# Kernel optimization log

Measured on AMD Instinct MI355X. Metric: run time of the kernel, lower is better.

## Reference

```python
import jax, jax.numpy as jnp
import numpy as np

N = 500_000   # active voxel sites
C = 128       # inplanes == outplanes
K = 4         # 2x2 submanifold filter offsets
EPS = 1e-4    # SCN BatchNorm default eps


def setup_inputs() -> dict:
    key = jax.random.key(0)
    ks = jax.random.split(key, 10)
    feat = jax.random.normal(ks[0], (N, C), jnp.float32)
    in_idx = jax.random.randint(ks[1], (K, N), 0, N, dtype=jnp.int32)
    out_idx = jax.random.randint(ks[2], (K, N), 0, N, dtype=jnp.int32)
    mask = jax.random.randint(ks[3], (K, N), 0, 2, dtype=jnp.int32)
    scale = 1.0 / np.sqrt(K * C)
    W1 = jax.random.normal(ks[4], (K, C, C), jnp.float32) * scale
    W2 = jax.random.normal(ks[5], (K, C, C), jnp.float32) * scale
    gamma1 = jnp.ones((C,), jnp.float32)
    beta1 = jnp.zeros((C,), jnp.float32)
    mean1 = jax.random.normal(ks[6], (C,), jnp.float32) * 0.1
    var1 = jax.random.uniform(ks[7], (C,), jnp.float32, 0.5, 1.5)
    gamma2 = jnp.ones((C,), jnp.float32)
    beta2 = jnp.zeros((C,), jnp.float32)
    mean2 = jax.random.normal(ks[8], (C,), jnp.float32) * 0.1
    var2 = jax.random.uniform(ks[9], (C,), jnp.float32, 0.5, 1.5)
    return dict(feat=feat, W1=W1, W2=W2, gamma1=gamma1, beta1=beta1,
                mean1=mean1, var1=var1, gamma2=gamma2, beta2=beta2,
                mean2=mean2, var2=var2, in_idx=in_idx, out_idx=out_idx, mask=mask)


def _subm_conv(feat, W, in_idx, out_idx, maskf):
    # rulebook gather -> GEMM -> scatter-add, one pass per kernel offset
    out = jnp.zeros((feat.shape[0], W.shape[-1]), feat.dtype)
    for k in range(W.shape[0]):  # K=4 fixed small offsets
        g = feat[in_idx[k]] * maskf[k][:, None]   # [N, Cin]
        out = out.at[out_idx[k]].add(g @ W[k])    # scatter to active sites
    return out


def _bn(x, gamma, beta, mean, var):
    return (x - mean) * jax.lax.rsqrt(var + EPS) * gamma + beta


def reference(feat, W1, W2, gamma1, beta1, mean1, var1,
              gamma2, beta2, mean2, var2, in_idx, out_idx, mask):
    maskf = mask.astype(feat.dtype)
    residual = feat                              # scn.Identity (stride=1)
    h = _subm_conv(feat, W1, in_idx, out_idx, maskf)
    h = jax.nn.relu(_bn(h, gamma1, beta1, mean1, var1))  # BatchNormReLU
    h = _subm_conv(h, W2, in_idx, out_idx, maskf)
    h = _bn(h, gamma2, beta2, mean2, var2)       # BatchNormalization
    return h + residual                          # AddTable
```

## Files before the change

kernel.cpp:

```cpp
#include <hip/hip_runtime.h>

#define CDIM 128
#define KOFF 4
#define EPS 1e-4f
#define SCAN_CHUNK 2048
#define ROWS 16
#define NBUF 4
#define NBLK 512
#define NTHR 512
#define CAPM (1 << 18)

typedef __attribute__((ext_vector_type(8))) short bf16x8;
typedef __attribute__((ext_vector_type(4))) float f32x4;

__device__ __forceinline__ unsigned short f2bf(float f) {
    unsigned int u = __builtin_bit_cast(unsigned int, f);
    u += 0x7fffu + ((u >> 16) & 1u);
    return (unsigned short)(u >> 16);
}
__device__ __forceinline__ float bf2f(unsigned short h) {
    unsigned int u = ((unsigned int)h) << 16;
    return __builtin_bit_cast(float, u);
}

__device__ __forceinline__ void gload_lds16(const void* g, void* l) {
    __builtin_amdgcn_global_load_lds(
        (const __attribute__((address_space(1))) void*)g,
        (__attribute__((address_space(3))) void*)l, 16, 0, 0);
}

__global__ __launch_bounds__(256) void wconv_kernel(
    const float* __restrict__ W1, const float* __restrict__ W2,
    short* __restrict__ W1t, short* __restrict__ W2t)
{
    int idx = blockIdx.x * 256 + threadIdx.x;
    if (idx >= KOFF * CDIM * CDIM) return;
    int ci = idx & (CDIM - 1);
    int co = (idx >> 7) & (CDIM - 1);
    int k  = idx >> 14;
    size_t src = (size_t)k * CDIM * CDIM + (size_t)ci * CDIM + co;
    W1t[idx] = (short)f2bf(W1[src]);
    W2t[idx] = (short)f2bf(W2[src]);
}

__global__ __launch_bounds__(256) void prep_kernel(
    const int* __restrict__ out_idx, const int* __restrict__ mask,
    int* __restrict__ cnt, const float* __restrict__ feat,
    short* __restrict__ fb, int n, size_t total8)
{
    if (blockIdx.y == KOFF) {
        size_t stride = (size_t)gridDim.x * 256;
        for (size_t i = (size_t)blockIdx.x * 256 + threadIdx.x; i < total8; i += stride) {
            float4 a = ((const float4*)feat)[i * 2];
            float4 b = ((const float4*)feat)[i * 2 + 1];
            bf16x8 v;
            v[0] = (short)f2bf(a.x); v[1] = (short)f2bf(a.y);
            v[2] = (short)f2bf(a.z); v[3] = (short)f2bf(a.w);
            v[4] = (short)f2bf(b.x); v[5] = (short)f2bf(b.y);
            v[6] = (short)f2bf(b.z); v[7] = (short)f2bf(b.w);
            ((bf16x8*)fb)[i] = v;
        }
    } else {
        int i = blockIdx.x * 256 + threadIdx.x;
        if (i >= n) return;
        int k = blockIdx.y;
        size_t s = (size_t)k * n + i;
        if (mask[s]) atomicAdd(&cnt[(size_t)out_idx[s] * KOFF + k], 1);
    }
}

__global__ __launch_bounds__(256) void scan_p1(
    const int* __restrict__ in, int* __restrict__ bsum, int* __restrict__ bsum2, int L)
{
    __shared__ int red[256], red2[256];
    int base = blockIdx.x * SCAN_CHUNK;
    int s = 0, m = 0;
    #pragma unroll
    for (int u = 0; u < 8; ++u) {
        int i = base + u * 256 + threadIdx.x;
        if (i < L) { int v = in[i]; s += v; m += (v >= 2); }
    }
    red[threadIdx.x] = s; red2[threadIdx.x] = m;
    __syncthreads();
    for (int d = 128; d > 0; d >>= 1) {
        if (threadIdx.x < d) {
            red[threadIdx.x]  += red[threadIdx.x + d];
            red2[threadIdx.x] += red2[threadIdx.x + d];
        }
        __syncthreads();
    }
    if (threadIdx.x == 0) { bsum[blockIdx.x] = red[0]; bsum2[blockIdx.x] = red2[0]; }
}

__global__ __launch_bounds__(1024) void scan_p2(
    int* __restrict__ bsum, int* __restrict__ bsum2, int NB)
{
    __shared__ int s[1024], s2[1024];
    int t = threadIdx.x;
    s[t]  = (t < NB) ? bsum[t]  : 0;
    s2[t] = (t < NB) ? bsum2[t] : 0;
    __syncthreads();
    for (int d = 1; d < 1024; d <<= 1) {
        int x = s[t], y = s2[t];
        if (t >= d) { x += s[t - d]; y += s2[t - d]; }
        __syncthreads();
        s[t] = x; s2[t] = y;
        __syncthreads();
    }
    if (t < NB) {
        bsum[t]  = (t == 0) ? 0 : s[t - 1];
        bsum2[t] = (t == 0) ? 0 : s2[t - 1];
    }
}

__global__ __launch_bounds__(256) void scan_p3(
    const int* __restrict__ cnt, const int* __restrict__ bsum,
    const int* __restrict__ bsum2, int* __restrict__ off_start,
    int* __restrict__ fcur, int* __restrict__ prim,
    int* __restrict__ mlist, int* __restrict__ nmulti, int L, int KN)
{
    __shared__ int ts[256], ms[256];
    int t = threadIdx.x;
    int base = blockIdx.x * SCAN_CHUNK + t * 8;
    int v[8]; int s = 0, m = 0;
    #pragma unroll
    for (int u = 0; u < 8; ++u) {
        int i = base + u;
        v[u] = (i < L) ? cnt[i] : 0;
        s += v[u]; m += (v[u] >= 2);
    }
    ts[t] = s; ms[t] = m;
    __syncthreads();
    for (int d = 1; d < 256; d <<= 1) {
        int x = ts[t], y = ms[t];
        if (t >= d) { x += ts[t - d]; y += ms[t - d]; }
        __syncthreads();
        ts[t] = x; ms[t] = y;
        __syncthreads();
    }
    int pre  = bsum[blockIdx.x]  + ((t == 0) ? 0 : ts[t - 1]);
    int mpre = bsum2[blockIdx.x] + ((t == 0) ? 0 : ms[t - 1]);
    #pragma unroll
    for (int u = 0; u < 8; ++u) {
        int i = base + u;
        if (i < L) {
            off_start[i] = pre;
            fcur[i] = pre;
            if (i < KN) {
                int c = v[u];
                if (c == 0) prim[i] = -1;
                else if (c >= 2) {
                    if (mpre < CAPM) { prim[i] = 0x40000000 | mpre; mlist[mpre] = i; }
                    else prim[i] = -1;
                }
            } else {
                nmulti[0] = mpre;
            }
            pre += v[u]; mpre += (v[u] >= 2);
        }
    }
}

__global__ __launch_bounds__(256) void fill_kernel(
    const int* __restrict__ out_idx, const int* __restrict__ in_idx,
    const int* __restrict__ mask, const int* __restrict__ cnt,
    int* __restrict__ fcur, int* __restrict__ ent, int* __restrict__ prim, int n)
{
    int i = blockIdx.x * 256 + threadIdx.x;
    if (i >= n) return;
    int k = blockIdx.y;
    size_t s = (size_t)k * n + i;
    if (mask[s]) {
        int j = out_idx[s];
        size_t b = (size_t)j * KOFF + k;
        int src = in_idx[s];
        if (cnt[b] == 1) prim[b] = src;
        else { int pos = atomicAdd(&fcur[b], 1); ent[pos] = src; }
    }
}

__global__ __launch_bounds__(256) void merge_kernel(
    const short* __restrict__ Xb, const int* __restrict__ off_start,
    const int* __restrict__ ent, const int* __restrict__ mlist,
    const int* __restrict__ nmulti, short* __restrict__ sumbuf)
{
    int nm = *nmulti; if (nm > CAPM) nm = CAPM;
    int grp  = (blockIdx.x * 256 + threadIdx.x) >> 5;
    int gl   = threadIdx.x & 31;
    int ngrp = (gridDim.x * 256) >> 5;
    for (int i = grp; i < nm; i += ngrp) {
        int b  = mlist[i];
        int e0 = off_start[b];
        int e1 = off_start[b + 1];
        float a0 = 0.f, a1 = 0.f, a2 = 0.f, a3 = 0.f;
        for (int e = e0; e < e1; ++e) {
            int src = ent[e];
            ushort4 v = *((const ushort4*)(Xb + (size_t)src * CDIM) + gl);
            a0 += bf2f(v.x); a1 += bf2f(v.y); a2 += bf2f(v.z); a3 += bf2f(v.w);
        }
        ushort4 o;
        o.x = f2bf(a0); o.y = f2bf(a1); o.z = f2bf(a2); o.w = f2bf(a3);
        *((ushort4*)(sumbuf + (size_t)i * CDIM) + gl) = o;
    }
}

template <int EPI>
__global__ __launch_bounds__(NTHR, 4) void conv_kernel(
    const short* __restrict__ Xb, const short* __restrict__ sumbuf,
    const short* __restrict__ Wt, const int* __restrict__ prim,
    const char* __restrict__ zpage,
    const float* __restrict__ gamma, const float* __restrict__ beta,
    const float* __restrict__ mean, const float* __restrict__ var,
    const float* __restrict__ feat, void* __restrict__ Yv,
    int n, int ntile, int tpb)
{
    const int t    = threadIdx.x;
    const int w    = t >> 6;
    const int lane = t & 63;

    __shared__ alignas(16) short As[NBUF][ROWS * 512];
    __shared__ alignas(16) float s_scale[CDIM], s_shift[CDIM];

    if (t < CDIM) {
        float sc = gamma[t] * rsqrtf(var[t] + EPS);
        s_scale[t] = sc;
        s_shift[t] = beta[t] - mean[t] * sc;
    }
    __syncthreads();

    int t0 = blockIdx.x * tpb;
    int t1 = min(t0 + tpb, ntile);
    if (t0 >= t1) return;

    const int q    = lane >> 4;
    const int p    = lane & 15;
    const int lrow = lane & 15;
    const int g2   = lane >> 4;
    const int col  = w * 16 + lrow;

    bf16x8 wfr[16];
    #pragma unroll
    for (int ks = 0; ks < 16; ++ks) {
        int k  = ks >> 2;
        int kk = ks & 3;
        wfr[ks] = *(const bf16x8*)(Wt + (size_t)k * CDIM * CDIM
                                   + (w * 16 + lrow) * CDIM + kk * 32 + g2 * 8);
    }

    auto LOADP = [&](int ti, int* pr) {
        int tc = (ti < t1) ? ti : (t1 - 1);
        int j0 = tc * ROWS;
        #pragma unroll
        for (int i = 0; i < 2; ++i)
            pr[i] = prim[(size_t)(j0 + w * 2 + i) * KOFF + q];
    };
    auto STAGE = [&](const int* pr, int buf) {
        #pragma unroll
        for (int i = 0; i < 2; ++i) {
            int jl = w * 2 + i;
            int boff = ((p ^ (jl & 7)) << 4);
            int pv = pr[i];
            const char* g;
            if (pv < 0)               g = zpage + boff;
            else if (pv & 0x40000000) g = (const char*)sumbuf + ((size_t)(pv & 0x3FFFFFFF) << 8) + boff;
            else                      g = (const char*)Xb + ((size_t)pv << 8) + boff;
            gload_lds16(g, (char*)As[buf] + jl * 1024);
        }
    };

    auto ITER = [&](int ti, int rb, int sb, const int* prS, int* prL, auto&& VMW) {
        STAGE(prS, sb);
        LOADP(ti + 4, prL);
        VMW();
        __builtin_amdgcn_s_barrier();
        __builtin_amdgcn_sched_barrier(0);

        f32x4 acc = (f32x4){0.f, 0.f, 0.f, 0.f};
        __builtin_amdgcn_s_setprio(1);
        #pragma unroll
        for (int ks = 0; ks < 16; ++ks) {
            int cb = ks * 4 + g2;
            bf16x8 a = *(const bf16x8*)(&As[rb][lrow * 512 + ((cb ^ (lrow & 7)) << 3)]);
            acc = __builtin_amdgcn_mfma_f32_16x16x32_bf16(a, wfr[ks], acc, 0, 0, 0);
        }
        __builtin_amdgcn_s_setprio(0);
        asm volatile("s_waitcnt lgkmcnt(0)" ::: "memory");
        __builtin_amdgcn_s_barrier();

        float* Ot = (float*)As[rb];
        #pragma unroll
        for (int jj = 0; jj < 4; ++jj)
            Ot[(g2 * 4 + jj) * 132 + col] = acc[jj];
        asm volatile("s_waitcnt lgkmcnt(0)" ::: "memory");
        __builtin_amdgcn_s_barrier();

        {
            int row = t >> 5, c4 = t & 31;
            int grow = ti * ROWS + row;
            if (grow < n) {
                float4 x  = *(const float4*)(Ot + row * 132 + c4 * 4);
                float4 sc = ((const float4*)s_scale)[c4];
                float4 sh = ((const float4*)s_shift)[c4];
                size_t go = (size_t)grow * 32 + c4;
                if (EPI == 0) {
                    ushort4 o;
                    o.x = f2bf(fmaxf(x.x * sc.x + sh.x, 0.f));
                    o.y = f2bf(fmaxf(x.y * sc.y + sh.y, 0.f));
                    o.z = f2bf(fmaxf(x.z * sc.z + sh.z, 0.f));
                    o.w = f2bf(fmaxf(x.w * sc.w + sh.w, 0.f));
                    ((ushort4*)Yv)[go] = o;
                } else {
                    float4 f = ((const float4*)feat)[go];
                    float4 r;
                    r.x = x.x * sc.x + sh.x + f.x;
                    r.y = x.y * sc.y + sh.y + f.y;
                    r.z = x.z * sc.z + sh.z + f.z;
                    r.w = x.w * sc.w + sh.w + f.w;
                    ((float4*)Yv)[go] = r;
                }
            }
        }
        asm volatile("s_waitcnt lgkmcnt(0)" ::: "memory");
        __builtin_amdgcn_s_barrier();
    };

    #define VMW_LIT(N0, N1)                                                     \
        [] {                                                                    \
            if (EPI == 0) asm volatile("s_waitcnt vmcnt(" #N0 ")" ::: "memory");\
            else          asm volatile("s_waitcnt vmcnt(" #N1 ")" ::: "memory");\
        }

    int p0[2], p1[2], p2[2], p3[2];
    LOADP(t0,     p0);
    LOADP(t0 + 1, p1);
    LOADP(t0 + 2, p2);
    STAGE(p0, 0);
    STAGE(p1, 1);
    STAGE(p2, 2);
    LOADP(t0 + 3, p3);

    ITER(t0 + 0, 0, 3, p3, p0, VMW_LIT(10, 10));
    if (t0 + 1 < t1) {
        ITER(t0 + 1, 1, 0, p0, p1, VMW_LIT(13, 14));
        if (t0 + 2 < t1) {
            ITER(t0 + 2, 2, 1, p1, p2, VMW_LIT(16, 18));
            if (t0 + 3 < t1) {
                ITER(t0 + 3, 3, 2, p2, p3, VMW_LIT(17, 20));
                for (int ti = t0 + 4; ti < t1; ti += 4) {
                    ITER(ti, 0, 3, p3, p0, VMW_LIT(17, 20));
                    if (ti + 1 >= t1) break;
                    ITER(ti + 1, 1, 0, p0, p1, VMW_LIT(17, 20));
                    if (ti + 2 >= t1) break;
                    ITER(ti + 2, 2, 1, p1, p2, VMW_LIT(17, 20));
                    if (ti + 3 >= t1) break;
                    ITER(ti + 3, 3, 2, p2, p3, VMW_LIT(17, 20));
                }
            }
        }
    }
    #undef VMW_LIT
}

extern "C" void kernel_launch(void* const* d_in, const int* in_sizes, int n_in,
                              void* d_out, int out_size, void* d_ws, size_t ws_size,
                              hipStream_t stream)
{
    const float* feat   = (const float*)d_in[0];
    const float* W1     = (const float*)d_in[1];
    const float* W2     = (const float*)d_in[2];
    const float* gamma1 = (const float*)d_in[3];
    const float* beta1  = (const float*)d_in[4];
    const float* mean1  = (const float*)d_in[5];
    const float* var1   = (const float*)d_in[6];
    const float* gamma2 = (const float*)d_in[7];
    const float* beta2  = (const float*)d_in[8];
    const float* mean2  = (const float*)d_in[9];
    const float* var2   = (const float*)d_in[10];
    const int* in_idx   = (const int*)d_in[11];
    const int* out_idx  = (const int*)d_in[12];
    const int* mask     = (const int*)d_in[13];

    const int n  = in_sizes[0] / CDIM;
    const int KN = KOFF * n;
    const int L  = KN + 1;
    const int NB = (L + SCAN_CHUNK - 1) / SCAN_CHUNK;
    const size_t nelem = (size_t)n * CDIM;

    auto alignup = [](size_t x) { return (x + 255) & ~(size_t)255; };
    char* p = (char*)d_ws;
    int*   cnt    = (int*)p;    p += alignup((size_t)L * 4);
    int*   offs   = (int*)p;    p += alignup((size_t)L * 4);
    int*   fcur   = (int*)p;    p += alignup((size_t)L * 4);
    int*   bsum   = (int*)p;    p += alignup(4096 * 4);
    int*   bsum2  = (int*)p;    p += alignup(4096 * 4);
    int*   ent    = (int*)p;    p += alignup((size_t)KN * 4);
    int*   prim   = (int*)p;    p += alignup((size_t)KN * 4);
    int*   mlist  = (int*)p;    p += alignup((size_t)CAPM * 4);
    int*   nmulti = (int*)p;    p += 256;
    short* W1t    = (short*)p;  p += alignup((size_t)KOFF * CDIM * CDIM * 2);
    short* W2t    = (short*)p;  p += alignup((size_t)KOFF * CDIM * CDIM * 2);
    char*  zpage  = p;          p += 256;
    short* sumbuf = (short*)p;  p += alignup((size_t)CAPM * CDIM * 2);
    short* h1b    = (short*)p;
    short* fb     = (short*)d_out;

    hipMemsetAsync(cnt, 0, (size_t)L * 4, stream);
    hipMemsetAsync(zpage, 0, 256, stream);
    wconv_kernel<<<(KOFF * CDIM * CDIM + 255) / 256, 256, 0, stream>>>(W1, W2, W1t, W2t);
    dim3 pg((n + 255) / 256, KOFF + 1);
    prep_kernel<<<pg, 256, 0, stream>>>(out_idx, mask, cnt, feat, fb, n, nelem / 8);
    scan_p1<<<NB, 256, 0, stream>>>(cnt, bsum, bsum2, L);
    scan_p2<<<1, 1024, 0, stream>>>(bsum, bsum2, NB);
    scan_p3<<<NB, 256, 0, stream>>>(cnt, bsum, bsum2, offs, fcur, prim, mlist, nmulti, L, KN);
    dim3 fg((n + 255) / 256, KOFF);
    fill_kernel<<<fg, 256, 0, stream>>>(out_idx, in_idx, mask, cnt, fcur, ent, prim, n);

    const int ntile = n / ROWS;
    const int tpb   = (ntile + NBLK - 1) / NBLK;

    merge_kernel<<<1024, 256, 0, stream>>>(fb, offs, ent, mlist, nmulti, sumbuf);
    conv_kernel<0><<<NBLK, NTHR, 0, stream>>>(
        fb, sumbuf, W1t, prim, zpage, gamma1, beta1, mean1, var1, nullptr, h1b, n, ntile, tpb);
    merge_kernel<<<1024, 256, 0, stream>>>(h1b, offs, ent, mlist, nmulti, sumbuf);
    conv_kernel<1><<<NBLK, NTHR, 0, stream>>>(
        h1b, sumbuf, W2t, prim, zpage, gamma2, beta2, mean2, var2, feat, d_out, n, ntile, tpb);
}
```

Measured before the change: 611.4 us.

## Fuse setup kernels, use decoupled look-back scan, and write conv epilogue directly

Weight conversion and zero-page init are folded into the prep kernel, and the three-pass scan is replaced by one single-pass decoupled look-back scan that uses an atomic block counter. The separate offset array is dropped because merge recovers entry ranges from fcur minus cnt. The conv epilogue now writes results straight from MFMA accumulators with the residual prefetched, skipping the LDS transpose and two barriers, and the vmcnt wait literals are retuned to match. This cuts kernel launches and LDS round trips, at the cost of spin-waiting in the scan and less coalesced per-column global stores.

```diff
diff --git a/kernel.cpp b/kernel.cpp
--- a/kernel.cpp
+++ b/kernel.cpp
@@ -29,24 +29,13 @@
         (__attribute__((address_space(3))) void*)l, 16, 0, 0);
 }
 
-__global__ __launch_bounds__(256) void wconv_kernel(
-    const float* __restrict__ W1, const float* __restrict__ W2,
-    short* __restrict__ W1t, short* __restrict__ W2t)
-{
-    int idx = blockIdx.x * 256 + threadIdx.x;
-    if (idx >= KOFF * CDIM * CDIM) return;
-    int ci = idx & (CDIM - 1);
-    int co = (idx >> 7) & (CDIM - 1);
-    int k  = idx >> 14;
-    size_t src = (size_t)k * CDIM * CDIM + (size_t)ci * CDIM + co;
-    W1t[idx] = (short)f2bf(W1[src]);
-    W2t[idx] = (short)f2bf(W2[src]);
-}
-
 __global__ __launch_bounds__(256) void prep_kernel(
     const int* __restrict__ out_idx, const int* __restrict__ mask,
     int* __restrict__ cnt, const float* __restrict__ feat,
-    short* __restrict__ fb, int n, size_t total8)
+    short* __restrict__ fb,
+    const float* __restrict__ W1, const float* __restrict__ W2,
+    short* __restrict__ W1t, short* __restrict__ W2t, int* __restrict__ zpage,
+    int n, size_t total8)
 {
     if (blockIdx.y == KOFF) {
         size_t stride = (size_t)gridDim.x * 256;
@@ -60,6 +49,16 @@
             v[6] = (short)f2bf(b.z); v[7] = (short)f2bf(b.w);
             ((bf16x8*)fb)[i] = v;
         }
+    } else if (blockIdx.y == KOFF + 1) {
+        if (blockIdx.x == 0 && threadIdx.x < 64) zpage[threadIdx.x] = 0;
+        int idx = blockIdx.x * 256 + threadIdx.x;
+        if (idx >= KOFF * CDIM * CDIM) return;
+        int ci = idx & (CDIM - 1);
+        int co = (idx >> 7) & (CDIM - 1);
+        int k  = idx >> 14;
+        size_t src = (size_t)k * CDIM * CDIM + (size_t)ci * CDIM + co;
+        W1t[idx] = (short)f2bf(W1[src]);
+        W2t[idx] = (short)f2bf(W2[src]);
     } else {
         int i = blockIdx.x * 256 + threadIdx.x;
         if (i >= n) return;
@@ -69,59 +68,25 @@
     }
 }
 
-__global__ __launch_bounds__(256) void scan_p1(
-    const int* __restrict__ in, int* __restrict__ bsum, int* __restrict__ bsum2, int L)
-{
-    __shared__ int red[256], red2[256];
-    int base = blockIdx.x * SCAN_CHUNK;
-    int s = 0, m = 0;
-    #pragma unroll
-    for (int u = 0; u < 8; ++u) {
-        int i = base + u * 256 + threadIdx.x;
-        if (i < L) { int v = in[i]; s += v; m += (v >= 2); }
-    }
-    red[threadIdx.x] = s; red2[threadIdx.x] = m;
+__device__ __forceinline__ unsigned long long lb_pack(int st, int s, int m) {
+    return ((unsigned long long)st << 62) |
+           ((unsigned long long)(unsigned)s << 24) |
+           (unsigned long long)(unsigned)m;
+}
+
+__global__ __launch_bounds__(256) void scan_lb_kernel(
+    const int* __restrict__ cnt, int* __restrict__ fcur, int* __restrict__ prim,
+    int* __restrict__ mlist, int* __restrict__ nmulti,
+    unsigned long long* __restrict__ agg, int* __restrict__ wgctr, int L, int KN)
+{
+    __shared__ int ts[256], ms[256];
+    __shared__ int s_bid, s_ps, s_pm;
+    int t = threadIdx.x;
+    if (t == 0) s_bid = atomicAdd(wgctr, 1);
     __syncthreads();
-    for (int d = 128; d > 0; d >>= 1) {
-        if (threadIdx.x < d) {
-            red[threadIdx.x]  += red[threadIdx.x + d];
-            red2[threadIdx.x] += red2[threadIdx.x + d];
-        }
-        __syncthreads();
-    }
-    if (threadIdx.x == 0) { bsum[blockIdx.x] = red[0]; bsum2[blockIdx.x] = red2[0]; }
-}
-
-__global__ __launch_bounds__(1024) void scan_p2(
-    int* __restrict__ bsum, int* __restrict__ bsum2, int NB)
-{
-    __shared__ int s[1024], s2[1024];
-    int t = threadIdx.x;
-    s[t]  = (t < NB) ? bsum[t]  : 0;
-    s2[t] = (t < NB) ? bsum2[t] : 0;
-    __syncthreads();
-    for (int d = 1; d < 1024; d <<= 1) {
-        int x = s[t], y = s2[t];
-        if (t >= d) { x += s[t - d]; y += s2[t - d]; }
-        __syncthreads();
-        s[t] = x; s2[t] = y;
-        __syncthreads();
-    }
-    if (t < NB) {
-        bsum[t]  = (t == 0) ? 0 : s[t - 1];
-        bsum2[t] = (t == 0) ? 0 : s2[t - 1];
-    }
-}
-
-__global__ __launch_bounds__(256) void scan_p3(
-    const int* __restrict__ cnt, const int* __restrict__ bsum,
-    const int* __restrict__ bsum2, int* __restrict__ off_start,
-    int* __restrict__ fcur, int* __restrict__ prim,
-    int* __restrict__ mlist, int* __restrict__ nmulti, int L, int KN)
-{
-    __shared__ int ts[256], ms[256];
-    int t = threadIdx.x;
-    int base = blockIdx.x * SCAN_CHUNK + t * 8;
+    const int bid = s_bid;
+    int base = bid * SCAN_CHUNK + t * 8;
+
     int v[8]; int s = 0, m = 0;
     #pragma unroll
     for (int u = 0; u < 8; ++u) {
@@ -138,13 +103,35 @@
         ts[t] = x; ms[t] = y;
         __syncthreads();
     }
-    int pre  = bsum[blockIdx.x]  + ((t == 0) ? 0 : ts[t - 1]);
-    int mpre = bsum2[blockIdx.x] + ((t == 0) ? 0 : ms[t - 1]);
+
+    if (t == 0) {
+        int bs = ts[255], bm = ms[255];
+        if (bid == 0) {
+            atomicExch(&agg[0], lb_pack(2, bs, bm));
+            s_ps = 0; s_pm = 0;
+        } else {
+            atomicExch(&agg[bid], lb_pack(1, bs, bm));
+            int exs = 0, exm = 0, pred = bid - 1;
+            while (true) {
+                unsigned long long x;
+                do { x = atomicAdd(&agg[pred], 0ULL); } while ((x >> 62) == 0ULL);
+                exm += (int)(x & 0xFFFFFFULL);
+                exs += (int)((x >> 24) & 0xFFFFFFFFULL);
+                if ((x >> 62) == 2ULL) break;
+                --pred;
+            }
+            atomicExch(&agg[bid], lb_pack(2, exs + bs, exm + bm));
+            s_ps = exs; s_pm = exm;
+        }
+    }
+    __syncthreads();
+
+    int pre  = s_ps + ((t == 0) ? 0 : ts[t - 1]);
+    int mpre = s_pm + ((t == 0) ? 0 : ms[t - 1]);
     #pragma unroll
     for (int u = 0; u < 8; ++u) {
         int i = base + u;
         if (i < L) {
-            off_start[i] = pre;
             fcur[i] = pre;
             if (i < KN) {
                 int c = v[u];
@@ -180,9 +167,10 @@
 }
 
 __global__ __launch_bounds__(256) void merge_kernel(
-    const short* __restrict__ Xb, const int* __restrict__ off_start,
-    const int* __restrict__ ent, const int* __restrict__ mlist,
-    const int* __restrict__ nmulti, short* __restrict__ sumbuf)
+    const short* __restrict__ Xb, const int* __restrict__ fcur,
+    const int* __restrict__ cnt, const int* __restrict__ ent,
+    const int* __restrict__ mlist, const int* __restrict__ nmulti,
+    short* __restrict__ sumbuf)
 {
     int nm = *nmulti; if (nm > CAPM) nm = CAPM;
     int grp  = (blockIdx.x * 256 + threadIdx.x) >> 5;
@@ -190,8 +178,8 @@
     int ngrp = (gridDim.x * 256) >> 5;
     for (int i = grp; i < nm; i += ngrp) {
         int b  = mlist[i];
-        int e0 = off_start[b];
-        int e1 = off_start[b + 1];
+        int e1 = fcur[b];
+        int e0 = e1 - cnt[b];
         float a0 = 0.f, a1 = 0.f, a2 = 0.f, a3 = 0.f;
         for (int e = e0; e < e1; ++e) {
             int src = ent[e];
@@ -237,6 +225,9 @@
     const int lrow = lane & 15;
     const int g2   = lane >> 4;
     const int col  = w * 16 + lrow;
+
+    const float csc = s_scale[col];
+    const float csh = s_shift[col];
 
     bf16x8 wfr[16];
     #pragma unroll
@@ -269,8 +260,15 @@
     };
 
     auto ITER = [&](int ti, int rb, int sb, const int* prS, int* prL, auto&& VMW) {
+        float fres[4];
+        if (EPI == 1) {
+            #pragma unroll
+            for (int jj = 0; jj < 4; ++jj)
+                fres[jj] = feat[(size_t)(ti * ROWS + g2 * 4 + jj) * CDIM + col];
+        }
         STAGE(prS, sb);
         LOADP(ti + 4, prL);
+        __builtin_amdgcn_sched_barrier(0);
         VMW();
         __builtin_amdgcn_s_barrier();
         __builtin_amdgcn_sched_barrier(0);
@@ -287,41 +285,22 @@
         asm volatile("s_waitcnt lgkmcnt(0)" ::: "memory");
         __builtin_amdgcn_s_barrier();
 
-        float* Ot = (float*)As[rb];
-        #pragma unroll
-        for (int jj = 0; jj < 4; ++jj)
-            Ot[(g2 * 4 + jj) * 132 + col] = acc[jj];
-        asm volatile("s_waitcnt lgkmcnt(0)" ::: "memory");
-        __builtin_amdgcn_s_barrier();
-
-        {
-            int row = t >> 5, c4 = t & 31;
-            int grow = ti * ROWS + row;
-            if (grow < n) {
-                float4 x  = *(const float4*)(Ot + row * 132 + c4 * 4);
-                float4 sc = ((const float4*)s_scale)[c4];
-                float4 sh = ((const float4*)s_shift)[c4];
-                size_t go = (size_t)grow * 32 + c4;
-                if (EPI == 0) {
-                    ushort4 o;
-                    o.x = f2bf(fmaxf(x.x * sc.x + sh.x, 0.f));
-                    o.y = f2bf(fmaxf(x.y * sc.y + sh.y, 0.f));
-                    o.z = f2bf(fmaxf(x.z * sc.z + sh.z, 0.f));
-                    o.w = f2bf(fmaxf(x.w * sc.w + sh.w, 0.f));
-                    ((ushort4*)Yv)[go] = o;
-                } else {
-                    float4 f = ((const float4*)feat)[go];
-                    float4 r;
-                    r.x = x.x * sc.x + sh.x + f.x;
-                    r.y = x.y * sc.y + sh.y + f.y;
-                    r.z = x.z * sc.z + sh.z + f.z;
-                    r.w = x.w * sc.w + sh.w + f.w;
-                    ((float4*)Yv)[go] = r;
-                }
+        if (EPI == 0) {
+            unsigned short* out = (unsigned short*)Yv;
+            #pragma unroll
+            for (int jj = 0; jj < 4; ++jj) {
+                int row = ti * ROWS + g2 * 4 + jj;
+                out[(size_t)row * CDIM + col] = f2bf(fmaxf(acc[jj] * csc + csh, 0.f));
             }
-        }
-        asm volatile("s_waitcnt lgkmcnt(0)" ::: "memory");
-        __builtin_amdgcn_s_barrier();
+        } else {
+            float* out = (float*)Yv;
+            #pragma unroll
+            for (int jj = 0; jj < 4; ++jj) {
+                int row = ti * ROWS + g2 * 4 + jj;
+                out[(size_t)row * CDIM + col] = acc[jj] * csc + csh + fres[jj];
+            }
+        }
+        __builtin_amdgcn_sched_barrier(0);
     };
 
     #define VMW_LIT(N0, N1)                                                     \
@@ -339,21 +318,21 @@
     STAGE(p2, 2);
     LOADP(t0 + 3, p3);
 
-    ITER(t0 + 0, 0, 3, p3, p0, VMW_LIT(10, 10));
+    ITER(t0 + 0, 0, 3, p3, p0, VMW_LIT(10, 14));
     if (t0 + 1 < t1) {
-        ITER(t0 + 1, 1, 0, p0, p1, VMW_LIT(13, 14));
+        ITER(t0 + 1, 1, 0, p0, p1, VMW_LIT(16, 24));
         if (t0 + 2 < t1) {
-            ITER(t0 + 2, 2, 1, p1, p2, VMW_LIT(16, 18));
+            ITER(t0 + 2, 2, 1, p1, p2, VMW_LIT(22, 34));
             if (t0 + 3 < t1) {
-                ITER(t0 + 3, 3, 2, p2, p3, VMW_LIT(17, 20));
+                ITER(t0 + 3, 3, 2, p2, p3, VMW_LIT(26, 38));
                 for (int ti = t0 + 4; ti < t1; ti += 4) {
-                    ITER(ti, 0, 3, p3, p0, VMW_LIT(17, 20));
+                    ITER(ti, 0, 3, p3, p0, VMW_LIT(26, 38));
                     if (ti + 1 >= t1) break;
-                    ITER(ti + 1, 1, 0, p0, p1, VMW_LIT(17, 20));
+                    ITER(ti + 1, 1, 0, p0, p1, VMW_LIT(26, 38));
                     if (ti + 2 >= t1) break;
-                    ITER(ti + 2, 2, 1, p1, p2, VMW_LIT(17, 20));
+                    ITER(ti + 2, 2, 1, p1, p2, VMW_LIT(26, 38));
                     if (ti + 3 >= t1) break;
-                    ITER(ti + 3, 3, 2, p2, p3, VMW_LIT(17, 20));
+                    ITER(ti + 3, 3, 2, p2, p3, VMW_LIT(26, 38));
                 }
             }
         }
@@ -389,39 +368,39 @@
     auto alignup = [](size_t x) { return (x + 255) & ~(size_t)255; };
     char* p = (char*)d_ws;
     int*   cnt    = (int*)p;    p += alignup((size_t)L * 4);
-    int*   offs   = (int*)p;    p += alignup((size_t)L * 4);
+    unsigned long long* agg = (unsigned long long*)p; p += alignup((size_t)NB * 8);
+    int*   wgctr  = (int*)p;    p += 256;
+    size_t zlen = (size_t)(p - (char*)d_ws);
     int*   fcur   = (int*)p;    p += alignup((size_t)L * 4);
-    int*   bsum   = (int*)p;    p += alignup(4096 * 4);
-    int*   bsum2  = (int*)p;    p += alignup(4096 * 4);
     int*   ent    = (int*)p;    p += alignup((size_t)KN * 4);
     int*   prim   = (int*)p;    p += alignup((size_t)KN * 4);
     int*   mlist  = (int*)p;    p += alignup((size_t)CAPM * 4);
     int*   nmulti = (int*)p;    p += 256;
     short* W1t    = (short*)p;  p += alignup((size_t)KOFF * CDIM * CDIM * 2);
     short* W2t    = (short*)p;  p += alignup((size_t)KOFF * CDIM * CDIM * 2);
-    char*  zpage  = p;          p += 256;
+    int*   zpage  = (int*)p;    p += 256;
     short* sumbuf = (short*)p;  p += alignup((size_t)CAPM * CDIM * 2);
     short* h1b    = (short*)p;
     short* fb     = (short*)d_out;
 
-    hipMemsetAsync(cnt, 0, (size_t)L * 4, stream);
-    hipMemsetAsync(zpage, 0, 256, stream);
-    wconv_kernel<<<(KOFF * CDIM * CDIM + 255) / 256, 256, 0, stream>>>(W1, W2, W1t, W2t);
-    dim3 pg((n + 255) / 256, KOFF + 1);
-    prep_kernel<<<pg, 256, 0, stream>>>(out_idx, mask, cnt, feat, fb, n, nelem / 8);
-    scan_p1<<<NB, 256, 0, stream>>>(cnt, bsum, bsum2, L);
-    scan_p2<<<1, 1024, 0, stream>>>(bsum, bsum2, NB);
-    scan_p3<<<NB, 256, 0, stream>>>(cnt, bsum, bsum2, offs, fcur, prim, mlist, nmulti, L, KN);
+    hipMemsetAsync(cnt, 0, zlen, stream);
+    dim3 pg((n + 255) / 256, KOFF + 2);
+    prep_kernel<<<pg, 256, 0, stream>>>(out_idx, mask, cnt, feat, fb,
+                                        W1, W2, W1t, W2t, zpage, n, nelem / 8);
+    scan_lb_kernel<<<NB, 256, 0, stream>>>(cnt, fcur, prim, mlist, nmulti,
+                                           agg, wgctr, L, KN);
     dim3 fg((n + 255) / 256, KOFF);
     fill_kernel<<<fg, 256, 0, stream>>>(out_idx, in_idx, mask, cnt, fcur, ent, prim, n);
 
     const int ntile = n / ROWS;
     const int tpb   = (ntile + NBLK - 1) / NBLK;
 
-    merge_kernel<<<1024, 256, 0, stream>>>(fb, offs, ent, mlist, nmulti, sumbuf);
+    merge_kernel<<<1024, 256, 0, stream>>>(fb, fcur, cnt, ent, mlist, nmulti, sumbuf);
     conv_kernel<0><<<NBLK, NTHR, 0, stream>>>(
-        fb, sumbuf, W1t, prim, zpage, gamma1, beta1, mean1, var1, nullptr, h1b, n, ntile, tpb);
-    merge_kernel<<<1024, 256, 0, stream>>>(h1b, offs, ent, mlist, nmulti, sumbuf);
+        fb, sumbuf, W1t, prim, (const char*)zpage, gamma1, beta1, mean1, var1,
+        nullptr, h1b, n, ntile, tpb);
+    merge_kernel<<<1024, 256, 0, stream>>>(h1b, fcur, cnt, ent, mlist, nmulti, sumbuf);
     conv_kernel<1><<<NBLK, NTHR, 0, stream>>>(
-        h1b, sumbuf, W2t, prim, zpage, gamma2, beta2, mean2, var2, feat, d_out, n, ntile, tpb);
-}
+        h1b, sumbuf, W2t, prim, (const char*)zpage, gamma2, beta2, mean2, var2,
+        feat, d_out, n, ntile, tpb);
+}
```

Measured after the change: 619.9 us. No clear change (+1.4%).
